# Kernel optimization log

Hardware: AMD Instinct MI355X
Metric: run time of the kernel (lower is better)

## Reference

```python
import jax, jax.numpy as jnp
import numpy as np

V, E, H, L = 32000, 1024, 1024, 2
B, T = 64, 256


def setup_inputs() -> dict:
    key = jax.random.key(0)
    ks = jax.random.split(key, 6)
    src = jax.random.randint(ks[0], (B, T), 0, V, dtype=jnp.int32)
    s_e = 1.0 / np.sqrt(H)
    emb = jax.random.normal(ks[1], (V, E), dtype=jnp.float32) * 0.02
    # stacked-layer LSTM params; layer 0 input = E == H so shapes are uniform
    W_ih = jax.random.uniform(ks[2], (L, 4 * H, H), dtype=jnp.float32, minval=-s_e, maxval=s_e)
    W_hh = jax.random.uniform(ks[3], (L, 4 * H, H), dtype=jnp.float32, minval=-s_e, maxval=s_e)
    b_ih = jax.random.uniform(ks[4], (L, 4 * H), dtype=jnp.float32, minval=-s_e, maxval=s_e)
    b_hh = jax.random.uniform(ks[5], (L, 4 * H), dtype=jnp.float32, minval=-s_e, maxval=s_e)
    return {"src": src, "emb": emb, "W_ih": W_ih, "W_hh": W_hh, "b_ih": b_ih, "b_hh": b_hh}


def _lstm_stack(embedded, W_ih, W_hh, b_ih, b_hh):
    # embedded: [B, T, E]
    Bsz = embedded.shape[0]
    h0 = jnp.zeros((L, Bsz, H), embedded.dtype)
    c0 = jnp.zeros((L, Bsz, H), embedded.dtype)

    def step(carry, x_t):
        h, c = carry  # each [L, B, H]
        x = x_t       # [B, E]
        new_h, new_c = [], []
        for l in range(L):
            gates = x @ W_ih[l].T + b_ih[l] + h[l] @ W_hh[l].T + b_hh[l]  # [B, 4H]
            i, f, g, o = jnp.split(gates, 4, axis=-1)
            c_t = jax.nn.sigmoid(f) * c[l] + jax.nn.sigmoid(i) * jnp.tanh(g)
            h_t = jax.nn.sigmoid(o) * jnp.tanh(c_t)
            new_h.append(h_t)
            new_c.append(c_t)
            x = h_t  # feed to next layer (dropout p=0)
        return (jnp.stack(new_h), jnp.stack(new_c)), x

    (h_n, c_n), outs = jax.lax.scan(step, (h0, c0), jnp.swapaxes(embedded, 0, 1))
    return jnp.swapaxes(outs, 0, 1), h_n, c_n  # [B,T,H], [L,B,H], [L,B,H]


def reference(src, emb, W_ih, W_hh, b_ih, b_hh):
    embedded = emb[src]  # [B, T, E]
    encoder_outputs, h_n, c_n = _lstm_stack(embedded, W_ih, W_hh, b_ih, b_hh)
    return encoder_outputs, (h_n, c_n)
```

## Files before the change

### kernel.cpp

```cpp
#include <hip/hip_runtime.h>
#include <hip/hip_bf16.h>

typedef __hip_bfloat16 bf16;
typedef __attribute__((ext_vector_type(8))) short s16x8;
typedef __attribute__((ext_vector_type(4))) float f32x4;
typedef __attribute__((ext_vector_type(4))) int   i32x4;

#define BATCH   64
#define SEQ     256
#define HID     1024
#define GATES   4096
#define NWG     256
#define THREADS 256
#define UNITS   8
#define NCOLS   32
#define ROWSTRIDE 2056
#define GSTRIDE 33
#define BH      (BATCH * HID)

#define H0_SLOTS 4
#define H1_SLOTS 2
#define FLAG_ELEMS ((size_t)6 * BH)
#define WS_BYTES  (FLAG_ELEMS * 2 + 34 * 128)

#define OUT_HN  ((size_t)BATCH * SEQ * HID)
#define OUT_CN  (OUT_HN + 2ull * BATCH * HID)

__device__ __forceinline__ short f2bf(float f) {
    unsigned int u = __builtin_bit_cast(unsigned int, f);
    u = (u + 0x7fffu + ((u >> 16) & 1u)) >> 16;
    return (short)u;
}

__device__ __forceinline__ s16x8 ldg16(const bf16* p) {
    i32x4 r;
    asm volatile("global_load_dwordx4 %0, %1, off sc0 sc1" : "=v"(r) : "v"(p));
    return __builtin_bit_cast(s16x8, r);
}

__device__ __forceinline__ void gemm_bt(const bf16* xrow, const bf16* s0, const bf16* s1,
                                        f32x4& a0, f32x4& a1)
{
    s16x8 ha[32];
#pragma unroll
    for (int kk = 0; kk < 32; ++kk) ha[kk] = ldg16(xrow + kk * 32);
    asm volatile("s_waitcnt vmcnt(0)");
    __builtin_amdgcn_sched_barrier(0);
#pragma unroll
    for (int kk = 0; kk < 32; ++kk) {
        s16x8 b0 = *(const s16x8*)(s0 + kk * 32);
        s16x8 b1 = *(const s16x8*)(s1 + kk * 32);
        a0 = __builtin_amdgcn_mfma_f32_16x16x32_bf16(ha[kk], b0, a0, 0, 0, 0);
        a1 = __builtin_amdgcn_mfma_f32_16x16x32_bf16(ha[kk], b1, a1, 0, 0, 0);
    }
}

__device__ __forceinline__ void wait16(unsigned int* base, int tid, int tgt) {
    if (tid < 16 && tgt > 0) {
        unsigned int* p = base + tid * 32;
        while ((int)__hip_atomic_load(p, __ATOMIC_RELAXED, __HIP_MEMORY_SCOPE_AGENT) < tgt)
            __builtin_amdgcn_s_sleep(1);
    }
    __syncthreads();
}

__global__ void ws_init(unsigned int* p, int n) {
    for (int i = blockIdx.x * blockDim.x + threadIdx.x; i < n; i += gridDim.x * blockDim.x)
        p[i] = 0u;
}

__global__ void __launch_bounds__(THREADS, 1)
lstm_enc(const int* __restrict__ src, const float* __restrict__ Wemb,
         const float* __restrict__ Wih, const float* __restrict__ Whh,
         const float* __restrict__ bih, const float* __restrict__ bhh,
         float* __restrict__ out, bf16* __restrict__ hbuf)
{
    __shared__ __align__(16) bf16 slab[NCOLS][ROWSTRIDE];
    __shared__ float gates[BATCH][GSTRIDE];
    __shared__ float bias[NCOLS];

    const int wg    = blockIdx.x;
    const int layer = wg >> 7;
    const int wgl   = wg & 127;
    const int j0    = wgl * UNITS;
    const int tid   = threadIdx.x;
    const int lane  = tid & 63;
    const int wave  = tid >> 6;
    const int m     = lane & 15;
    const int kq    = (lane >> 4) * 8;
    const int b_a   = wave * 16 + m;

    for (int r = 0; r < NCOLS; ++r) {
        int g = r >> 3, u = r & 7;
        size_t grow = (size_t)layer * GATES * HID + (size_t)(g * HID + j0 + u) * HID;
        int k = tid * 8;
        const float* s = (k < HID) ? (Wih + grow + k) : (Whh + grow + (k - HID));
        s16x8 v;
#pragma unroll
        for (int j = 0; j < 8; ++j) v[j] = f2bf(s[j]);
        *(s16x8*)&slab[r][k] = v;
    }
    if (tid < NCOLS) {
        int g = tid >> 3, u = tid & 7;
        int off = layer * GATES + g * HID + j0 + u;
        bias[tid] = bih[off] + bhh[off];
    }
    __syncthreads();

    bf16* h0 = hbuf;
    bf16* h1 = hbuf + H0_SLOTS * BH;
    unsigned int* flags = (unsigned int*)(hbuf + FLAG_ELEMS);
    unsigned int* grp = flags + (16 * layer + (wgl >> 3)) * 32;
    unsigned int* g0  = flags;
    unsigned int* g1  = flags + 16 * 32;

    const int bb = tid >> 2;
    const int u0 = (tid & 3) * 2;
    float c_lo = 0.f, c_hi = 0.f;

    int sv = (layer == 0) ? src[b_a * SEQ] : 0;

    for (int t = 0; t < SEQ; ++t) {
        f32x4 acc0 = {0.f, 0.f, 0.f, 0.f};
        f32x4 acc1 = {0.f, 0.f, 0.f, 0.f};

        if (layer == 0) {
            const float* xF = Wemb + (size_t)sv * HID + kq;
            if (t + 1 < SEQ) sv = src[b_a * SEQ + t + 1];
#pragma unroll
            for (int c = 0; c < 4; ++c) {
                f32x4 xv[16];
#pragma unroll
                for (int i = 0; i < 8; ++i) {
                    const float* p = xF + (c * 8 + i) * 32;
                    xv[2 * i]     = *(const f32x4*)p;
                    xv[2 * i + 1] = *(const f32x4*)(p + 4);
                }
#pragma unroll
                for (int i = 0; i < 8; ++i) {
                    const int k = (c * 8 + i) * 32 + kq;
                    s16x8 af;
#pragma unroll
                    for (int j = 0; j < 4; ++j) {
                        af[j]     = f2bf(xv[2 * i][j]);
                        af[4 + j] = f2bf(xv[2 * i + 1][j]);
                    }
                    s16x8 b0 = *(const s16x8*)&slab[m][k];
                    s16x8 b1 = *(const s16x8*)&slab[16 + m][k];
                    acc0 = __builtin_amdgcn_mfma_f32_16x16x32_bf16(af, b0, acc0, 0, 0, 0);
                    acc1 = __builtin_amdgcn_mfma_f32_16x16x32_bf16(af, b1, acc1, 0, 0, 0);
                }
            }
            wait16(g0, tid, 8 * t);
            gemm_bt(h0 + (size_t)((t - 1) & (H0_SLOTS - 1)) * BH + b_a * HID + kq,
                    &slab[m][HID + kq], &slab[16 + m][HID + kq], acc0, acc1);
        } else {
            wait16(g0, tid, 8 * (t + 1));
            gemm_bt(h0 + (size_t)(t & (H0_SLOTS - 1)) * BH + b_a * HID + kq,
                    &slab[m][kq], &slab[16 + m][kq], acc0, acc1);
            wait16(g1, tid, 8 * t);
            gemm_bt(h1 + (size_t)((t - 1) & (H1_SLOTS - 1)) * BH + b_a * HID + kq,
                    &slab[m][HID + kq], &slab[16 + m][HID + kq], acc0, acc1);
        }

        const int rowg = wave * 16 + (lane >> 4) * 4;
#pragma unroll
        for (int r = 0; r < 4; ++r) {
            gates[rowg + r][m]      = acc0[r];
            gates[rowg + r][16 + m] = acc1[r];
        }

        if (layer == 0) wait16(g1, tid, 8 * (t - 3));
        else            __syncthreads();

        {
            float gi0 = gates[bb][u0]      + bias[u0];
            float gi1 = gates[bb][u0 + 1]  + bias[u0 + 1];
            float gf0 = gates[bb][u0 + 8]  + bias[u0 + 8];
            float gf1 = gates[bb][u0 + 9]  + bias[u0 + 9];
            float gg0 = gates[bb][u0 + 16] + bias[u0 + 16];
            float gg1 = gates[bb][u0 + 17] + bias[u0 + 17];
            float go0 = gates[bb][u0 + 24] + bias[u0 + 24];
            float go1 = gates[bb][u0 + 25] + bias[u0 + 25];
            float si0 = 1.f / (1.f + __expf(-gi0)), si1 = 1.f / (1.f + __expf(-gi1));
            float sf0 = 1.f / (1.f + __expf(-gf0)), sf1 = 1.f / (1.f + __expf(-gf1));
            float so0 = 1.f / (1.f + __expf(-go0)), so1 = 1.f / (1.f + __expf(-go1));
            float tg0 = tanhf(gg0), tg1 = tanhf(gg1);
            c_lo = sf0 * c_lo + si0 * tg0;
            c_hi = sf1 * c_hi + si1 * tg1;
            float h_lo = so0 * tanhf(c_lo);
            float h_hi = so1 * tanhf(c_hi);

            bf16* hw = ((layer == 0) ? h0 + (size_t)(t & (H0_SLOTS - 1)) * BH
                                     : h1 + (size_t)(t & (H1_SLOTS - 1)) * BH);
            unsigned int hp = (unsigned int)(unsigned short)f2bf(h_lo) |
                              ((unsigned int)(unsigned short)f2bf(h_hi) << 16);
            __hip_atomic_store((unsigned int*)(hw + bb * HID + j0 + u0), hp,
                               __ATOMIC_RELAXED, __HIP_MEMORY_SCOPE_AGENT);
            if (layer == 1) {
                float2 hv = make_float2(h_lo, h_hi);
                *(float2*)(out + ((size_t)bb * SEQ + t) * HID + j0 + u0) = hv;
            }
            if (t == SEQ - 1) {
                size_t o = ((size_t)layer * BATCH + bb) * HID + j0 + u0;
                *(float2*)(out + OUT_HN + o) = make_float2(h_lo, h_hi);
                *(float2*)(out + OUT_CN + o) = make_float2(c_lo, c_hi);
            }
        }
        __syncthreads();
        if (tid == 0)
            __hip_atomic_fetch_add(grp, 1u, __ATOMIC_RELAXED, __HIP_MEMORY_SCOPE_AGENT);
    }
}

extern "C" void kernel_launch(void* const* d_in, const int* in_sizes, int n_in,
                              void* d_out, int out_size, void* d_ws, size_t ws_size,
                              hipStream_t stream) {
    const int*   src  = (const int*)d_in[0];
    const float* emb  = (const float*)d_in[1];
    const float* W_ih = (const float*)d_in[2];
    const float* W_hh = (const float*)d_in[3];
    const float* b_ih = (const float*)d_in[4];
    const float* b_hh = (const float*)d_in[5];
    float* out  = (float*)d_out;
    bf16*  hbuf = (bf16*)d_ws;

    unsigned int* wsp = (unsigned int*)d_ws;
    int n = (int)(WS_BYTES / 4);
    ws_init<<<256, 256, 0, stream>>>(wsp, n);

    void* args[] = {&src, &emb, &W_ih, &W_hh, &b_ih, &b_hh, &out, &hbuf};
    hipLaunchCooperativeKernel((void*)lstm_enc, dim3(NWG), dim3(THREADS),
                               args, 0, stream);
}
```

Measured before the change: 3.837 ms.

## Replace grouped atomic counters with per-WG flags and pipeline h loads

Per-group fetch_add counters are replaced by one flag per workgroup, written as a plain store of t+1. Each of the 256 threads polls one WG's flag, so the layer-0 and layer-1 waits merge into a single barrier. The recurrent-state GEMM now issues its global loads in stages with partial waitcnts, so MFMAs overlap the remaining loads, and it drops sc1 in favour of occasional agent acquire fences. This cuts synchronisation latency per timestep but relies on relaxed ordering and periodic fences for correctness, which carries a memory-visibility risk.

```diff
diff --git a/kernel.cpp b/kernel.cpp
--- a/kernel.cpp
+++ b/kernel.cpp
@@ -21,7 +21,7 @@
 #define H0_SLOTS 4
 #define H1_SLOTS 2
 #define FLAG_ELEMS ((size_t)6 * BH)
-#define WS_BYTES  (FLAG_ELEMS * 2 + 34 * 128)
+#define WS_BYTES  (FLAG_ELEMS * 2 + 256 * 4)
 
 #define OUT_HN  ((size_t)BATCH * SEQ * HID)
 #define OUT_CN  (OUT_HN + 2ull * BATCH * HID)
@@ -32,36 +32,56 @@
     return (short)u;
 }
 
-__device__ __forceinline__ s16x8 ldg16(const bf16* p) {
-    i32x4 r;
-    asm volatile("global_load_dwordx4 %0, %1, off sc0 sc1" : "=v"(r) : "v"(p));
-    return __builtin_bit_cast(s16x8, r);
-}
+__device__ __forceinline__ void st8(void* p, float lo, float hi) {
+    union { float f[2]; unsigned long long u; } v;
+    v.f[0] = lo; v.f[1] = hi;
+    __hip_atomic_store((unsigned long long*)p, v.u, __ATOMIC_RELAXED, __HIP_MEMORY_SCOPE_AGENT);
+}
+
+#define MM8(B0) \
+    _Pragma("unroll") \
+    for (int kk = (B0); kk < (B0) + 8; ++kk) { \
+        s16x8 b0 = *(const s16x8*)(s0 + kk * 32); \
+        s16x8 b1 = *(const s16x8*)(s1 + kk * 32); \
+        s16x8 av = __builtin_bit_cast(s16x8, h[kk]); \
+        a0 = __builtin_amdgcn_mfma_f32_16x16x32_bf16(av, b0, a0, 0, 0, 0); \
+        a1 = __builtin_amdgcn_mfma_f32_16x16x32_bf16(av, b1, a1, 0, 0, 0); \
+    }
 
 __device__ __forceinline__ void gemm_bt(const bf16* xrow, const bf16* s0, const bf16* s1,
                                         f32x4& a0, f32x4& a1)
 {
-    s16x8 ha[32];
-#pragma unroll
-    for (int kk = 0; kk < 32; ++kk) ha[kk] = ldg16(xrow + kk * 32);
-    asm volatile("s_waitcnt vmcnt(0)");
-    __builtin_amdgcn_sched_barrier(0);
-#pragma unroll
-    for (int kk = 0; kk < 32; ++kk) {
-        s16x8 b0 = *(const s16x8*)(s0 + kk * 32);
-        s16x8 b1 = *(const s16x8*)(s1 + kk * 32);
-        a0 = __builtin_amdgcn_mfma_f32_16x16x32_bf16(ha[kk], b0, a0, 0, 0, 0);
-        a1 = __builtin_amdgcn_mfma_f32_16x16x32_bf16(ha[kk], b1, a1, 0, 0, 0);
-    }
-}
-
-__device__ __forceinline__ void wait16(unsigned int* base, int tid, int tgt) {
-    if (tid < 16 && tgt > 0) {
-        unsigned int* p = base + tid * 32;
+    i32x4 h[32];
+#define LD(i, OFF) asm volatile("global_load_dwordx4 %0, %1, off offset:" OFF " sc0" \
+                                : "=v"(h[i]) : "v"(xrow))
+    LD(0, "0");    LD(1, "64");   LD(2, "128");  LD(3, "192");
+    LD(4, "256");  LD(5, "320");  LD(6, "384");  LD(7, "448");
+    LD(8, "512");  LD(9, "576");  LD(10, "640"); LD(11, "704");
+    LD(12, "768"); LD(13, "832"); LD(14, "896"); LD(15, "960");
+    LD(16, "1024"); LD(17, "1088"); LD(18, "1152"); LD(19, "1216");
+    LD(20, "1280"); LD(21, "1344"); LD(22, "1408"); LD(23, "1472");
+    asm volatile("s_waitcnt vmcnt(16)"); __builtin_amdgcn_sched_barrier(0);
+    MM8(0)
+    LD(24, "1536"); LD(25, "1600"); LD(26, "1664"); LD(27, "1728");
+    LD(28, "1792"); LD(29, "1856"); LD(30, "1920"); LD(31, "1984");
+    asm volatile("s_waitcnt vmcnt(16)"); __builtin_amdgcn_sched_barrier(0);
+    MM8(8)
+    asm volatile("s_waitcnt vmcnt(8)");  __builtin_amdgcn_sched_barrier(0);
+    MM8(16)
+    asm volatile("s_waitcnt vmcnt(0)");  __builtin_amdgcn_sched_barrier(0);
+    MM8(24)
+#undef LD
+}
+
+__device__ __forceinline__ void wait_dual(unsigned int* flags, int tid, int tgtA, int tgtB) {
+    const int tgt = (tid < 128) ? tgtA : tgtB;
+    if (tgt > 0) {
+        unsigned int* p = flags + tid;
         while ((int)__hip_atomic_load(p, __ATOMIC_RELAXED, __HIP_MEMORY_SCOPE_AGENT) < tgt)
             __builtin_amdgcn_s_sleep(1);
     }
     __syncthreads();
+    asm volatile("" ::: "memory");
 }
 
 __global__ void ws_init(unsigned int* p, int n) {
@@ -107,12 +127,11 @@
     }
     __syncthreads();
 
+    __builtin_amdgcn_fence(__ATOMIC_ACQUIRE, "agent");
+
     bf16* h0 = hbuf;
     bf16* h1 = hbuf + H0_SLOTS * BH;
     unsigned int* flags = (unsigned int*)(hbuf + FLAG_ELEMS);
-    unsigned int* grp = flags + (16 * layer + (wgl >> 3)) * 32;
-    unsigned int* g0  = flags;
-    unsigned int* g1  = flags + 16 * 32;
 
     const int bb = tid >> 2;
     const int u0 = (tid & 3) * 2;
@@ -151,14 +170,20 @@
                     acc1 = __builtin_amdgcn_mfma_f32_16x16x32_bf16(af, b1, acc1, 0, 0, 0);
                 }
             }
-            wait16(g0, tid, 8 * t);
+            wait_dual(flags, tid, t, t - 3);
+        } else {
+            wait_dual(flags, tid, t + 1, t);
+        }
+
+        if (((t + (wg >> 3)) & 7) == 0)
+            __builtin_amdgcn_fence(__ATOMIC_ACQUIRE, "agent");
+
+        if (layer == 0) {
             gemm_bt(h0 + (size_t)((t - 1) & (H0_SLOTS - 1)) * BH + b_a * HID + kq,
                     &slab[m][HID + kq], &slab[16 + m][HID + kq], acc0, acc1);
         } else {
-            wait16(g0, tid, 8 * (t + 1));
             gemm_bt(h0 + (size_t)(t & (H0_SLOTS - 1)) * BH + b_a * HID + kq,
                     &slab[m][kq], &slab[16 + m][kq], acc0, acc1);
-            wait16(g1, tid, 8 * t);
             gemm_bt(h1 + (size_t)((t - 1) & (H1_SLOTS - 1)) * BH + b_a * HID + kq,
                     &slab[m][HID + kq], &slab[16 + m][HID + kq], acc0, acc1);
         }
@@ -169,9 +194,7 @@
             gates[rowg + r][m]      = acc0[r];
             gates[rowg + r][16 + m] = acc1[r];
         }
-
-        if (layer == 0) wait16(g1, tid, 8 * (t - 3));
-        else            __syncthreads();
+        __syncthreads();
 
         {
             float gi0 = gates[bb][u0]      + bias[u0];
@@ -197,19 +220,19 @@
                               ((unsigned int)(unsigned short)f2bf(h_hi) << 16);
             __hip_atomic_store((unsigned int*)(hw + bb * HID + j0 + u0), hp,
                                __ATOMIC_RELAXED, __HIP_MEMORY_SCOPE_AGENT);
-            if (layer == 1) {
-                float2 hv = make_float2(h_lo, h_hi);
-                *(float2*)(out + ((size_t)bb * SEQ + t) * HID + j0 + u0) = hv;
-            }
+            if (layer == 1)
+                st8(out + ((size_t)bb * SEQ + t) * HID + j0 + u0, h_lo, h_hi);
             if (t == SEQ - 1) {
                 size_t o = ((size_t)layer * BATCH + bb) * HID + j0 + u0;
-                *(float2*)(out + OUT_HN + o) = make_float2(h_lo, h_hi);
-                *(float2*)(out + OUT_CN + o) = make_float2(c_lo, c_hi);
+                st8(out + OUT_HN + o, h_lo, h_hi);
+                st8(out + OUT_CN + o, c_lo, c_hi);
             }
         }
         __syncthreads();
+        asm volatile("" ::: "memory");
         if (tid == 0)
-            __hip_atomic_fetch_add(grp, 1u, __ATOMIC_RELAXED, __HIP_MEMORY_SCOPE_AGENT);
+            __hip_atomic_store(flags + wg, (unsigned int)(t + 1),
+                               __ATOMIC_RELAXED, __HIP_MEMORY_SCOPE_AGENT);
     }
 }
 
```

New measurement: 3.876 ms. No clear change (+1.0%).
